# Optimization experiments

Measured on AMD Instinct MI355X. Metric: run time of the kernel, lower is better.

## Reference

```python
import jax, jax.numpy as jnp
import numpy as np

NO_TRANS = -10000.0
B, S, T = 512, 1024, 64
START, STOP = 1, 2


def setup_inputs() -> dict:
    key = jax.random.key(0)
    k1, k2, k3, k4 = jax.random.split(key, 4)
    feats = jax.random.normal(k1, (B, S, T), dtype=jnp.float32)
    tags = jax.random.randint(k2, (B, S), 3, T)  # avoid pad/start/stop tags
    lengths = jax.random.randint(k3, (B,), 1, S + 1)
    masks = (jnp.arange(S)[None, :] < lengths[:, None]).astype(jnp.float32)
    transitions = jax.random.normal(k4, (T, T), dtype=jnp.float32) * 0.1
    # replicate the constrained init from __init__ (transitions[next, prev])
    transitions = (transitions
                   .at[START, :].set(NO_TRANS)   # nothing transitions into START
                   .at[:, STOP].set(NO_TRANS)    # nothing transitions out of STOP
                   .at[:, 0].set(NO_TRANS)
                   .at[0, :].set(NO_TRANS))
    return {"feats": feats, "tags": tags, "lengths": lengths, "masks": masks,
            "transitions": transitions, "start_idx": START, "stop_idx": STOP}


def reference(feats, tags, lengths, masks, transitions, start_idx, stop_idx):
    """CRF negative log-likelihood per sequence: log Z (forward algorithm) - gold path score.
    feats: [B,S,T] emissions, transitions: [T,T] (next, prev)."""
    Bsz, Slen, Tsz = feats.shape

    # ---- forward algorithm (log-partition), batched lax.scan over time ----
    init = jnp.full((Bsz, Tsz), NO_TRANS, dtype=feats.dtype).at[:, start_idx].set(0.0)

    def step(fv, emit):  # fv: [B,T] (prev alphas), emit: [B,T]
        # next_tag_var[b, next, prev] = fv[b, prev] + trans[next, prev] + emit[b, next]
        nv = jax.scipy.special.logsumexp(
            fv[:, None, :] + transitions[None, :, :] + emit[:, :, None], axis=2)
        return nv, nv

    _, all_fv = jax.lax.scan(step, init, jnp.swapaxes(feats, 0, 1))  # [S,B,T]
    # pick forward var at the last valid position of each sequence
    fv_final = all_fv[lengths - 1, jnp.arange(Bsz)]                  # [B,T]
    alpha = jax.scipy.special.logsumexp(fv_final + transitions[stop_idx][None, :], axis=1)

    # ---- gold path score (vectorized _score_sentence_batch) ----
    tags_ext = jnp.concatenate(
        [jnp.full((Bsz, 1), start_idx, dtype=tags.dtype), tags], axis=1)  # [B,S+1]
    tn, tc = tags_ext[:, 1:], tags_ext[:, :-1]                            # [B,S]
    trans_sc = transitions[tn, tc] * masks                                # [B,S]
    emit_sc = jnp.take_along_axis(feats, tn[:, :, None], axis=2)[..., 0] * masks
    ends = jnp.take_along_axis(tags_ext, lengths[:, None], axis=1)[:, 0]  # tag at last valid step
    gold = trans_sc.sum(axis=1) + emit_sc.sum(axis=1) + transitions[stop_idx, ends]

    return alpha - gold  # per-sequence NLL, shape [B]
```

## Files before the change

### kernel.cpp

```cpp
#include <hip/hip_runtime.h>


#define TT 64

__device__ __forceinline__ float readlane_f(float v, int lane) {
  return __builtin_bit_cast(float, __builtin_amdgcn_readlane(__builtin_bit_cast(int, v), lane));
}

#define DECLW(a,b_,c,d_) float w##a, w##b_, w##c, w##d_;
#define LOADW(a,b_,c,d_,off)                                              \
  {                                                                       \
    float4 r = *reinterpret_cast<const float4*>(trans + lane * TT + off); \
    w##a = __expf(r.x);                                                   \
    w##b_ = __expf(r.y);                                                  \
    w##c = __expf(r.z);                                                   \
    w##d_ = __expf(r.w);                                                  \
  }
#define FMAG(a,b_,c,d_)                    \
  a0 = fmaf(w##a, readlane_f(E, a), a0);   \
  a1 = fmaf(w##b_, readlane_f(E, b_), a1); \
  a2 = fmaf(w##c, readlane_f(E, c), a2);   \
  a3 = fmaf(w##d_, readlane_f(E, d_), a3);

#define MATVEC(accname)                                        \
  float a0 = 0.f, a1 = 0.f, a2 = 0.f, a3 = 0.f;                \
  FMAG(0, 1, 2, 3) FMAG(4, 5, 6, 7)                            \
  FMAG(8, 9, 10, 11) FMAG(12, 13, 14, 15)                      \
  FMAG(16, 17, 18, 19) FMAG(20, 21, 22, 23)                    \
  FMAG(24, 25, 26, 27) FMAG(28, 29, 30, 31)                    \
  FMAG(32, 33, 34, 35) FMAG(36, 37, 38, 39)                    \
  FMAG(40, 41, 42, 43) FMAG(44, 45, 46, 47)                    \
  FMAG(48, 49, 50, 51) FMAG(52, 53, 54, 55)                    \
  FMAG(56, 57, 58, 59) FMAG(60, 61, 62, 63)                    \
  float accname = (a0 + a1) + (a2 + a3);

#define RENORM()                                                                      \
  {                                                                                   \
    unsigned rb = (unsigned)__builtin_amdgcn_readlane(__builtin_bit_cast(int, E), 3); \
    int k = (int)((rb >> 23) & 0xFFu) - 127;                                          \
    C += k;                                                                           \
    E *= __builtin_bit_cast(float, (unsigned)(127 - k) << 23);                        \
  }

#define STEP(J, SBASE)                     \
  {                                        \
    float ecur = e##J;                     \
    MATVEC(acc);                           \
    E = ecur * acc;                        \
    e##J = __expf(f##J);                   \
    int pidx = (SBASE) + (J) + 16;         \
    pidx = pidx < S ? pidx : S - 1;        \
    f##J = fb[(size_t)TT * pidx];          \
  }

__global__ __launch_bounds__(64, 1) void crf_fwd_kernel(
    const float* __restrict__ feats, const int* __restrict__ tags,
    const int* __restrict__ lengths, const float* __restrict__ trans,
    const int* __restrict__ p_start, const int* __restrict__ p_stop,
    float* __restrict__ out, int B, int S) {
  const int lane = threadIdx.x;
  const int b = blockIdx.x;
  if (b >= B) return;

  __shared__ float s_trans[TT * TT];
  for (int i = lane * 4; i < TT * TT; i += 64 * 4) {
    *reinterpret_cast<float4*>(&s_trans[i]) =
        *reinterpret_cast<const float4*>(trans + i);
  }
  __syncthreads();

  const int start = *p_start;
  const int stop = *p_stop;
  const int len = lengths[b];

  DECLW(0, 1, 2, 3) DECLW(4, 5, 6, 7) DECLW(8, 9, 10, 11) DECLW(12, 13, 14, 15)
  DECLW(16, 17, 18, 19) DECLW(20, 21, 22, 23) DECLW(24, 25, 26, 27) DECLW(28, 29, 30, 31)
  DECLW(32, 33, 34, 35) DECLW(36, 37, 38, 39) DECLW(40, 41, 42, 43) DECLW(44, 45, 46, 47)
  DECLW(48, 49, 50, 51) DECLW(52, 53, 54, 55) DECLW(56, 57, 58, 59) DECLW(60, 61, 62, 63)

  LOADW(0, 1, 2, 3, 0) LOADW(4, 5, 6, 7, 4)
  LOADW(8, 9, 10, 11, 8) LOADW(12, 13, 14, 15, 12)
  LOADW(16, 17, 18, 19, 16) LOADW(20, 21, 22, 23, 20)
  LOADW(24, 25, 26, 27, 24) LOADW(28, 29, 30, 31, 28)
  LOADW(32, 33, 34, 35, 32) LOADW(36, 37, 38, 39, 36)
  LOADW(40, 41, 42, 43, 40) LOADW(44, 45, 46, 47, 44)
  LOADW(48, 49, 50, 51, 48) LOADW(52, 53, 54, 55, 52)
  LOADW(56, 57, 58, 59, 56) LOADW(60, 61, 62, 63, 60)

  float ws = __expf(trans[stop * TT + lane]);

  const float* fbase = feats + (size_t)b * S * TT;
  const float* fb = fbase + lane;
  const int* tb = tags + (size_t)b * S;

  float E = (lane == start) ? 1.0f : 0.0f;
  int C = 0;

#define PRIME(J)                                            \
  float e##J = __expf(fb[(size_t)TT * ((J) < S ? (J) : S - 1)]); \
  float f##J = fb[(size_t)TT * (((J) + 8) < S ? ((J) + 8) : S - 1)];
  PRIME(0) PRIME(1) PRIME(2) PRIME(3)
  PRIME(4) PRIME(5) PRIME(6) PRIME(7)
#undef PRIME

  int s = 0;
#pragma unroll 1
  for (; s + 8 <= len; s += 8) {
    STEP(0, s) STEP(1, s) STEP(2, s) STEP(3, s) RENORM();
    STEP(4, s) STEP(5, s) STEP(6, s) STEP(7, s) RENORM();
  }
#pragma unroll 1
  for (; s < len; ++s) {
    float ecur = __expf(fb[(size_t)TT * s]);
    MATVEC(acc);
    E = ecur * acc;
    RENORM();
  }

  float v = E * ws;
#pragma unroll
  for (int off = 32; off >= 1; off >>= 1) v += __shfl_xor(v, off, 64);
  float alpha = __logf(v) + (float)C * 0.6931471805599453f;

  float gs = 0.0f;
#pragma unroll 1
  for (int s0 = 0; s0 < len; s0 += 64) {
    int si = s0 + lane;
    if (si < len) {
      int t = tb[si];
      int tp = (si == 0) ? start : tb[si - 1];
      gs += s_trans[t * TT + tp] + fbase[(size_t)si * TT + t];
    }
  }
#pragma unroll
  for (int off = 32; off >= 1; off >>= 1) gs += __shfl_xor(gs, off, 64);
  int tend = tb[len - 1];
  float gold = gs + s_trans[stop * TT + tend];

  if (lane == 0) out[b] = alpha - gold;
}

extern "C" void kernel_launch(void* const* d_in, const int* in_sizes, int n_in,
                              void* d_out, int out_size, void* d_ws, size_t ws_size,
                              hipStream_t stream) {
  const float* feats = (const float*)d_in[0];
  const int* tags = (const int*)d_in[1];
  const int* lengths = (const int*)d_in[2];
  const float* trans = (const float*)d_in[4];
  const int* p_start = (const int*)d_in[5];
  const int* p_stop = (const int*)d_in[6];
  float* out = (float*)d_out;

  int B = in_sizes[2];
  int S = in_sizes[1] / B;
  crf_fwd_kernel<<<B, 64, 0, stream>>>(feats, tags, lengths, trans,
                                       p_start, p_stop, out, B, S);
}
```

Baseline: 418.5 us.

## Split CRF forward matvec across four waves with LDS-exchanged alphas

Each sequence now runs on a 256-thread block instead of one 64-lane wave. Each thread holds a 16-element slice of a transition row. The 64x64 matvec per timestep is done as partial dot products reduced with cross-lane shuffles, and the alpha vector is double-buffered in shared memory with a block barrier every step. The goal is to cut the serial per-step latency of the old 64 readlane+FMA chain, at the cost of a __syncthreads per timestep and LDS traffic. Renormalisation is folded into the step, and the first timestep is peeled out as an initial vector.

After: 390.4 us. -6.7%, faster.

```diff
diff --git a/kernel.cpp b/kernel.cpp
--- a/kernel.cpp
+++ b/kernel.cpp
@@ -3,67 +3,24 @@
 
 #define TT 64
 
-__device__ __forceinline__ float readlane_f(float v, int lane) {
-  return __builtin_bit_cast(float, __builtin_amdgcn_readlane(__builtin_bit_cast(int, v), lane));
-}
-
-#define DECLW(a,b_,c,d_) float w##a, w##b_, w##c, w##d_;
-#define LOADW(a,b_,c,d_,off)                                              \
-  {                                                                       \
-    float4 r = *reinterpret_cast<const float4*>(trans + lane * TT + off); \
-    w##a = __expf(r.x);                                                   \
-    w##b_ = __expf(r.y);                                                  \
-    w##c = __expf(r.z);                                                   \
-    w##d_ = __expf(r.w);                                                  \
-  }
-#define FMAG(a,b_,c,d_)                    \
-  a0 = fmaf(w##a, readlane_f(E, a), a0);   \
-  a1 = fmaf(w##b_, readlane_f(E, b_), a1); \
-  a2 = fmaf(w##c, readlane_f(E, c), a2);   \
-  a3 = fmaf(w##d_, readlane_f(E, d_), a3);
-
-#define MATVEC(accname)                                        \
-  float a0 = 0.f, a1 = 0.f, a2 = 0.f, a3 = 0.f;                \
-  FMAG(0, 1, 2, 3) FMAG(4, 5, 6, 7)                            \
-  FMAG(8, 9, 10, 11) FMAG(12, 13, 14, 15)                      \
-  FMAG(16, 17, 18, 19) FMAG(20, 21, 22, 23)                    \
-  FMAG(24, 25, 26, 27) FMAG(28, 29, 30, 31)                    \
-  FMAG(32, 33, 34, 35) FMAG(36, 37, 38, 39)                    \
-  FMAG(40, 41, 42, 43) FMAG(44, 45, 46, 47)                    \
-  FMAG(48, 49, 50, 51) FMAG(52, 53, 54, 55)                    \
-  FMAG(56, 57, 58, 59) FMAG(60, 61, 62, 63)                    \
-  float accname = (a0 + a1) + (a2 + a3);
-
-#define RENORM()                                                                      \
-  {                                                                                   \
-    unsigned rb = (unsigned)__builtin_amdgcn_readlane(__builtin_bit_cast(int, E), 3); \
-    int k = (int)((rb >> 23) & 0xFFu) - 127;                                          \
-    C += k;                                                                           \
-    E *= __builtin_bit_cast(float, (unsigned)(127 - k) << 23);                        \
-  }
-
-#define STEP(J, SBASE)                     \
-  {                                        \
-    float ecur = e##J;                     \
-    MATVEC(acc);                           \
-    E = ecur * acc;                        \
-    e##J = __expf(f##J);                   \
-    int pidx = (SBASE) + (J) + 16;         \
-    pidx = pidx < S ? pidx : S - 1;        \
-    f##J = fb[(size_t)TT * pidx];          \
-  }
-
-__global__ __launch_bounds__(64, 1) void crf_fwd_kernel(
+__global__ __launch_bounds__(256, 2) void crf_fwd_kernel(
     const float* __restrict__ feats, const int* __restrict__ tags,
     const int* __restrict__ lengths, const float* __restrict__ trans,
     const int* __restrict__ p_start, const int* __restrict__ p_stop,
     float* __restrict__ out, int B, int S) {
-  const int lane = threadIdx.x;
+  const int tid = threadIdx.x;
+  const int lane = tid & 63;
+  const int w = tid >> 6;
+  const int cg = lane >> 4;
+  const int li = lane & 15;
+  const int r = w * 16 + li;
   const int b = blockIdx.x;
-  if (b >= B) return;
 
   __shared__ float s_trans[TT * TT];
-  for (int i = lane * 4; i < TT * TT; i += 64 * 4) {
+  __shared__ __align__(16) float s_E[2][TT];
+  __shared__ float s_part[4];
+
+  for (int i = tid * 4; i < TT * TT; i += 256 * 4) {
     *reinterpret_cast<float4*>(&s_trans[i]) =
         *reinterpret_cast<const float4*>(trans + i);
   }
@@ -73,59 +30,109 @@
   const int stop = *p_stop;
   const int len = lengths[b];
 
-  DECLW(0, 1, 2, 3) DECLW(4, 5, 6, 7) DECLW(8, 9, 10, 11) DECLW(12, 13, 14, 15)
-  DECLW(16, 17, 18, 19) DECLW(20, 21, 22, 23) DECLW(24, 25, 26, 27) DECLW(28, 29, 30, 31)
-  DECLW(32, 33, 34, 35) DECLW(36, 37, 38, 39) DECLW(40, 41, 42, 43) DECLW(44, 45, 46, 47)
-  DECLW(48, 49, 50, 51) DECLW(52, 53, 54, 55) DECLW(56, 57, 58, 59) DECLW(60, 61, 62, 63)
-
-  LOADW(0, 1, 2, 3, 0) LOADW(4, 5, 6, 7, 4)
-  LOADW(8, 9, 10, 11, 8) LOADW(12, 13, 14, 15, 12)
-  LOADW(16, 17, 18, 19, 16) LOADW(20, 21, 22, 23, 20)
-  LOADW(24, 25, 26, 27, 24) LOADW(28, 29, 30, 31, 28)
-  LOADW(32, 33, 34, 35, 32) LOADW(36, 37, 38, 39, 36)
-  LOADW(40, 41, 42, 43, 40) LOADW(44, 45, 46, 47, 44)
-  LOADW(48, 49, 50, 51, 48) LOADW(52, 53, 54, 55, 52)
-  LOADW(56, 57, 58, 59, 56) LOADW(60, 61, 62, 63, 60)
-
-  float ws = __expf(trans[stop * TT + lane]);
+  float q0, q1, q2, q3, q4, q5, q6, q7, q8, q9, q10, q11, q12, q13, q14, q15;
+  {
+    const float* wr = s_trans + r * TT + cg * 16;
+    float4 t0 = *reinterpret_cast<const float4*>(wr + 0);
+    float4 t1 = *reinterpret_cast<const float4*>(wr + 4);
+    float4 t2 = *reinterpret_cast<const float4*>(wr + 8);
+    float4 t3 = *reinterpret_cast<const float4*>(wr + 12);
+    q0 = __expf(t0.x); q1 = __expf(t0.y); q2 = __expf(t0.z); q3 = __expf(t0.w);
+    q4 = __expf(t1.x); q5 = __expf(t1.y); q6 = __expf(t1.z); q7 = __expf(t1.w);
+    q8 = __expf(t2.x); q9 = __expf(t2.y); q10 = __expf(t2.z); q11 = __expf(t2.w);
+    q12 = __expf(t3.x); q13 = __expf(t3.y); q14 = __expf(t3.z); q15 = __expf(t3.w);
+  }
+  float ws_e = __expf(s_trans[stop * TT + lane]);
 
   const float* fbase = feats + (size_t)b * S * TT;
-  const float* fb = fbase + lane;
+  const float* fbr = fbase + r;
   const int* tb = tags + (size_t)b * S;
 
-  float E = (lane == start) ? 1.0f : 0.0f;
+  {
+    float iv = __expf(fbase[r]) * __expf(s_trans[r * TT + start]);
+    if (cg == 0) s_E[0][r] = iv;
+  }
   int C = 0;
+  int buf = 0;
+  __syncthreads();
 
-#define PRIME(J)                                            \
-  float e##J = __expf(fb[(size_t)TT * ((J) < S ? (J) : S - 1)]); \
-  float f##J = fb[(size_t)TT * (((J) + 8) < S ? ((J) + 8) : S - 1)];
+#define PRIME(J)                                                               \
+  float e##J = __expf(fbr[(size_t)TT * ((1 + (J)) < S ? (1 + (J)) : S - 1)]);  \
+  float f##J = fbr[(size_t)TT * ((9 + (J)) < S ? (9 + (J)) : S - 1)];
   PRIME(0) PRIME(1) PRIME(2) PRIME(3)
   PRIME(4) PRIME(5) PRIME(6) PRIME(7)
 #undef PRIME
 
-  int s = 0;
+#define MATVEC16(SUM, XB)                                                      \
+  float4 x0 = *reinterpret_cast<const float4*>((XB) + cg * 16 + 0);            \
+  float4 x1 = *reinterpret_cast<const float4*>((XB) + cg * 16 + 4);            \
+  float4 x2 = *reinterpret_cast<const float4*>((XB) + cg * 16 + 8);            \
+  float4 x3 = *reinterpret_cast<const float4*>((XB) + cg * 16 + 12);           \
+  float a0 = q0 * x0.x; float a1 = q1 * x0.y;                                  \
+  float a2 = q2 * x0.z; float a3 = q3 * x0.w;                                  \
+  a0 = fmaf(q4, x1.x, a0); a1 = fmaf(q5, x1.y, a1);                            \
+  a2 = fmaf(q6, x1.z, a2); a3 = fmaf(q7, x1.w, a3);                            \
+  a0 = fmaf(q8, x2.x, a0); a1 = fmaf(q9, x2.y, a1);                            \
+  a2 = fmaf(q10, x2.z, a2); a3 = fmaf(q11, x2.w, a3);                          \
+  a0 = fmaf(q12, x3.x, a0); a1 = fmaf(q13, x3.y, a1);                          \
+  a2 = fmaf(q14, x3.z, a2); a3 = fmaf(q15, x3.w, a3);                          \
+  float SUM = (a0 + a1) + (a2 + a3);                                           \
+  SUM += __shfl_xor(SUM, 16, 64);                                              \
+  SUM += __shfl_xor(SUM, 32, 64);
+
+#define STEP(J, SBASE, RN)                                                     \
+  {                                                                            \
+    const float* Eb = s_E[buf];                                               \
+    MATVEC16(sum, Eb);                                                         \
+    float En;                                                                  \
+    if (RN) {                                                                  \
+      unsigned rb = __builtin_bit_cast(unsigned, Eb[3]);                       \
+      int k = (int)((rb >> 23) & 0xFFu) - 127;                                 \
+      C += k;                                                                  \
+      float sc = __builtin_bit_cast(float, (unsigned)(127 - k) << 23);         \
+      En = e##J * sum * sc;                                                    \
+    } else {                                                                   \
+      En = e##J * sum;                                                         \
+    }                                                                          \
+    if (cg == 0) s_E[buf ^ 1][r] = En;                                         \
+    e##J = __expf(f##J);                                                       \
+    int pidx = (SBASE) + (J) + 16;                                             \
+    pidx = pidx < S ? pidx : S - 1;                                            \
+    f##J = fbr[(size_t)TT * pidx];                                             \
+    buf ^= 1;                                                                  \
+    __syncthreads();                                                           \
+  }
+
+  int s = 1;
 #pragma unroll 1
   for (; s + 8 <= len; s += 8) {
-    STEP(0, s) STEP(1, s) STEP(2, s) STEP(3, s) RENORM();
-    STEP(4, s) STEP(5, s) STEP(6, s) STEP(7, s) RENORM();
+    STEP(0, s, 0) STEP(1, s, 0) STEP(2, s, 0) STEP(3, s, 1)
+    STEP(4, s, 0) STEP(5, s, 0) STEP(6, s, 0) STEP(7, s, 1)
   }
 #pragma unroll 1
   for (; s < len; ++s) {
-    float ecur = __expf(fb[(size_t)TT * s]);
-    MATVEC(acc);
-    E = ecur * acc;
-    RENORM();
+    const float* Eb = s_E[buf];
+    MATVEC16(sum, Eb);
+    unsigned rb = __builtin_bit_cast(unsigned, Eb[3]);
+    int k = (int)((rb >> 23) & 0xFFu) - 127;
+    C += k;
+    float sc = __builtin_bit_cast(float, (unsigned)(127 - k) << 23);
+    float ecur = __expf(fbr[(size_t)TT * s]);
+    float En = ecur * sum * sc;
+    if (cg == 0) s_E[buf ^ 1][r] = En;
+    buf ^= 1;
+    __syncthreads();
   }
 
-  float v = E * ws;
+  float v = s_E[buf][lane] * ws_e;
 #pragma unroll
   for (int off = 32; off >= 1; off >>= 1) v += __shfl_xor(v, off, 64);
   float alpha = __logf(v) + (float)C * 0.6931471805599453f;
 
   float gs = 0.0f;
 #pragma unroll 1
-  for (int s0 = 0; s0 < len; s0 += 64) {
-    int si = s0 + lane;
+  for (int s0 = 0; s0 < len; s0 += 256) {
+    int si = s0 + tid;
     if (si < len) {
       int t = tb[si];
       int tp = (si == 0) ? start : tb[si - 1];
@@ -134,10 +141,13 @@
   }
 #pragma unroll
   for (int off = 32; off >= 1; off >>= 1) gs += __shfl_xor(gs, off, 64);
-  int tend = tb[len - 1];
-  float gold = gs + s_trans[stop * TT + tend];
-
-  if (lane == 0) out[b] = alpha - gold;
+  if (lane == 0) s_part[w] = gs;
+  __syncthreads();
+  if (tid == 0) {
+    float gold = (s_part[0] + s_part[1]) + (s_part[2] + s_part[3]) +
+                 s_trans[stop * TT + tb[len - 1]];
+    out[b] = alpha - gold;
+  }
 }
 
 extern "C" void kernel_launch(void* const* d_in, const int* in_sizes, int n_in,
@@ -153,6 +163,6 @@
 
   int B = in_sizes[2];
   int S = in_sizes[1] / B;
-  crf_fwd_kernel<<<B, 64, 0, stream>>>(feats, tags, lengths, trans,
-                                       p_start, p_stop, out, B, S);
+  crf_fwd_kernel<<<B, 256, 0, stream>>>(feats, tags, lengths, trans,
+                                        p_start, p_stop, out, B, S);
 }
```
